# Kernel optimization log

Measured on AMD Instinct MI355X. Metric: run time of the kernel, lower is better.

The kernel has to match this reference:

```python
import jax, jax.numpy as jnp
import numpy as np

B, S, HID, H = 4, 2048, 1024, 8
D = HID // H  # per-head dim = 128


def setup_inputs() -> dict:
    key = jax.random.key(0)
    ks = jax.random.split(key, 8)
    q = jax.random.normal(ks[0], (B, S, HID), dtype=jnp.float32)
    k = jax.random.normal(ks[1], (B, S, HID), dtype=jnp.float32)
    v = jax.random.normal(ks[2], (B, S, HID), dtype=jnp.float32)
    mask = jax.random.randint(ks[3], (B, S), 0, 2, dtype=jnp.int32)  # 1 = masked key
    # Linear(hidden, hidden, bias=False) weights, stored [in, out] so y = x @ W
    xavier = lambda kk: jax.random.uniform(kk, (HID, HID), jnp.float32,
                                           -np.sqrt(6.0 / (2 * HID)), np.sqrt(6.0 / (2 * HID)))
    return {"q": q, "k": k, "v": v, "mask": mask,
            "Wq": xavier(ks[4]), "Wk": xavier(ks[5]), "Wv": xavier(ks[6]), "Wo": xavier(ks[7])}


def reference(q, k, v, mask, Wq, Wk, Wv, Wo):
    scale = D ** -0.5
    # project and split heads: [B,S,HID] -> [B,H,S,D]
    qq = (q @ Wq).reshape(B, S, H, D).transpose(0, 2, 1, 3) * scale
    kk = (k @ Wk).reshape(B, S, H, D).transpose(0, 2, 1, 3)
    vv = (v @ Wv).reshape(B, S, H, D).transpose(0, 2, 1, 3)
    # scores [B,H,Sq,Sk]; mask broadcasts over heads and query rows (key padding)
    scores = jnp.einsum('bhqd,bhkd->bhqk', qq, kk)
    scores = jnp.where(mask.astype(bool)[:, None, None, :], jnp.float32(-1e9), scores)
    attn = jax.nn.softmax(scores, axis=-1)  # dropout_rate=0 (eval) -> identity
    ctx = jnp.einsum('bhqk,bhkd->bhqd', attn, vv)
    out = ctx.transpose(0, 2, 1, 3).reshape(B, S, HID) @ Wo
    return out, attn
```

## Files before the change

kernel.cpp:

```cpp
#include <hip/hip_runtime.h>
#include <hip/hip_bf16.h>

#define HIDN 1024
#define NH   8
#define DH   128
#define BB   4
#define SS   2048

typedef __bf16 bf16;
typedef bf16 bf16x4 __attribute__((ext_vector_type(4)));
typedef bf16 bf16x8 __attribute__((ext_vector_type(8)));
typedef float f32x4 __attribute__((ext_vector_type(4)));

static __device__ inline f32x4 mfma16(bf16x8 a, bf16x8 b, f32x4 c) {
    return __builtin_amdgcn_mfma_f32_16x16x32_bf16(a, b, c, 0, 0, 0);
}

static __device__ inline void gload_lds16(const void* g, void* l) {
    __builtin_amdgcn_global_load_lds(
        (const __attribute__((address_space(1))) unsigned int*)g,
        (__attribute__((address_space(3))) unsigned int*)l, 16, 0, 0);
}

__global__ void cvt_kernel(const float* __restrict__ q, const float* __restrict__ k,
                           const float* __restrict__ v,
                           bf16* __restrict__ qo, bf16* __restrict__ ko, bf16* __restrict__ vo) {
    const float* src = blockIdx.y == 0 ? q : blockIdx.y == 1 ? k : v;
    bf16* dst = blockIdx.y == 0 ? qo : blockIdx.y == 1 ? ko : vo;
    const size_t n = (size_t)BB * SS * HIDN;
    for (size_t i = ((size_t)blockIdx.x * blockDim.x + threadIdx.x) * 8; i < n;
         i += (size_t)gridDim.x * blockDim.x * 8) {
        float4 a = *(const float4*)&src[i];
        float4 b = *(const float4*)&src[i + 4];
        bf16x8 o = {(bf16)a.x, (bf16)a.y, (bf16)a.z, (bf16)a.w,
                    (bf16)b.x, (bf16)b.y, (bf16)b.z, (bf16)b.w};
        *(bf16x8*)&dst[i] = o;
    }
}

__global__ void wconv_kernel(const float* __restrict__ W0, const float* __restrict__ W1,
                             const float* __restrict__ W2, const float* __restrict__ W3,
                             bf16* __restrict__ O) {
    const float* W = blockIdx.z == 0 ? W0 : blockIdx.z == 1 ? W1 : blockIdx.z == 2 ? W2 : W3;
    bf16* WT = O + (size_t)blockIdx.z * HIDN * HIDN;
    int nb = blockIdx.x * 64;
    int kb = blockIdx.y * 64;
    int t = threadIdx.x;
    __shared__ bf16 tile[64][72];
    {
        int r = t >> 2, cp = (t & 3) * 16;
        #pragma unroll
        for (int j = 0; j < 16; j += 4) {
            float4 val = *(const float4*)&W[(size_t)(kb + r) * HIDN + nb + cp + j];
            tile[r][cp + j + 0] = (bf16)val.x;
            tile[r][cp + j + 1] = (bf16)val.y;
            tile[r][cp + j + 2] = (bf16)val.z;
            tile[r][cp + j + 3] = (bf16)val.w;
        }
    }
    __syncthreads();
    {
        int n = t >> 2, kp = (t & 3) * 16;
        bf16 o[16];
        #pragma unroll
        for (int j = 0; j < 16; ++j) o[j] = tile[kp + j][n];
        #pragma unroll
        for (int j = 0; j < 2; ++j)
            *(bf16x8*)&WT[(size_t)(nb + n) * HIDN + kb + kp + j * 8] = *(bf16x8*)&o[j * 8];
    }
}

template <typename CT>
__global__ __launch_bounds__(256, 2)
void gemm_bt_kernel(const bf16* __restrict__ A, const bf16* __restrict__ Bt,
                    CT* __restrict__ C, float alpha) {
    __shared__ bf16 Asm[128 * 64];
    __shared__ bf16 Bsm[128 * 64];
    int orig = blockIdx.x + blockIdx.y * gridDim.x;
    int virt = (orig & 7) * 64 + (orig >> 3);
    int bm = (virt & 63) * 128;
    int bn = (virt >> 6) * 128;
    int t = threadIdx.x;
    int wave = t >> 6, lane = t & 63;
    int wr = wave >> 1, wc = wave & 1;
    int lr = lane & 15, lg = lane >> 4;
    f32x4 acc[4][4] = {};
    for (int k0 = 0; k0 < HIDN; k0 += 64) {
        #pragma unroll
        for (int i = 0; i < 4; ++i) {
            int o = i * 4096 + wave * 1024 + lane * 16;
            int r = o >> 7, cb = o & 127;
            int cbs = cb ^ ((r & 7) << 4);
            gload_lds16(&A[(size_t)(bm + r) * HIDN + k0 + (cbs >> 1)],
                        (char*)Asm + i * 4096 + wave * 1024);
            gload_lds16(&Bt[(size_t)(bn + r) * HIDN + k0 + (cbs >> 1)],
                        (char*)Bsm + i * 4096 + wave * 1024);
        }
        asm volatile("s_waitcnt vmcnt(0)" ::: "memory");
        __syncthreads();
        #pragma unroll
        for (int kd = 0; kd < 2; ++kd) {
            bf16x8 af[4], bfr[4];
            #pragma unroll
            for (int mi = 0; mi < 4; ++mi) {
                int row = wr * 64 + mi * 16 + lr;
                int cb = (kd * 64 + lg * 16) ^ ((row & 7) << 4);
                af[mi] = *(const bf16x8*)((const char*)Asm + row * 128 + cb);
            }
            #pragma unroll
            for (int ni = 0; ni < 4; ++ni) {
                int row = wc * 64 + ni * 16 + lr;
                int cb = (kd * 64 + lg * 16) ^ ((row & 7) << 4);
                bfr[ni] = *(const bf16x8*)((const char*)Bsm + row * 128 + cb);
            }
            #pragma unroll
            for (int mi = 0; mi < 4; ++mi)
                #pragma unroll
                for (int ni = 0; ni < 4; ++ni)
                    acc[mi][ni] = mfma16(af[mi], bfr[ni], acc[mi][ni]);
        }
        __syncthreads();
    }
    #pragma unroll
    for (int mi = 0; mi < 4; ++mi)
        #pragma unroll
        for (int ni = 0; ni < 4; ++ni)
            #pragma unroll
            for (int r = 0; r < 4; ++r) {
                int row = bm + wr * 64 + mi * 16 + lg * 4 + r;
                int col = bn + wc * 64 + ni * 16 + lr;
                C[(size_t)row * HIDN + col] = (CT)(acc[mi][ni][r] * alpha);
            }
}

__global__ void vt_kernel(const bf16* __restrict__ vv, bf16* __restrict__ vvT) {
    int st = blockIdx.x;
    int bh = blockIdx.y;
    int b = bh >> 3, h = bh & 7;
    int t = threadIdx.x;
    __shared__ bf16 tile[64][136];
    {
        int r = t >> 2, part = (t & 3) * 32;
        #pragma unroll
        for (int j = 0; j < 4; ++j)
            *(bf16x8*)&tile[r][part + j * 8] =
                *(const bf16x8*)&vv[((size_t)b * SS + st * 64 + r) * HIDN + h * DH + part + j * 8];
    }
    __syncthreads();
    {
        int d = t >> 1, kh = (t & 1) * 32;
        bf16 o[32];
        #pragma unroll
        for (int j = 0; j < 32; ++j) o[j] = tile[kh + j][d];
        #pragma unroll
        for (int j = 0; j < 4; ++j)
            *(bf16x8*)&vvT[((size_t)bh * DH + d) * SS + st * 64 + kh + j * 8] = *(bf16x8*)&o[j * 8];
    }
}

static __device__ inline void stage_k(const bf16* kbase, int kt, bf16* Ksm, int wave, int lane) {
    #pragma unroll
    for (int i = 0; i < 8; ++i) {
        int o = i * 4096 + wave * 1024 + lane * 16;
        int r = o >> 8, cb = o & 255;
        int cbs = cb ^ ((r & 7) << 4);
        gload_lds16(&kbase[(size_t)(kt * 128 + r) * HIDN + (cbs >> 1)],
                    (char*)Ksm + i * 4096 + wave * 1024);
    }
    asm volatile("s_waitcnt vmcnt(0)" ::: "memory");
}

static __device__ inline bf16x8 read_k(const bf16* Ksm, int row, int cstart_bytes) {
    int cb = cstart_bytes ^ ((row & 7) << 4);
    return *(const bf16x8*)((const char*)Ksm + row * 256 + cb);
}

__global__ __launch_bounds__(256, 2)
void attn_stats_kernel(const bf16* __restrict__ qq, const bf16* __restrict__ kk,
                       const int* __restrict__ mask,
                       float* __restrict__ mrow, float* __restrict__ lrow) {
    int orig = blockIdx.x + blockIdx.y * gridDim.x;
    int virt = (orig & 7) * 64 + (orig >> 3);
    int qt = virt & 15, bh = virt >> 4;
    int b = bh >> 3, h = bh & 7;
    int t = threadIdx.x;
    int wave = t >> 6, lane = t & 63;
    int wr = wave >> 1, wc = wave & 1;
    int lr = lane & 15, lg = lane >> 4;

    __shared__ bf16 Ksm[128 * 128];
    __shared__ float sm[2][128], sl[2][128], runm[128], runl[128];
    if (t < 128) { runm[t] = -3.4e38f; runl[t] = 0.f; }

    const bf16* qbase = qq + (size_t)b * SS * HIDN + h * DH;
    const bf16* kbase = kk + (size_t)b * SS * HIDN + h * DH;
    const int* mbase = mask + b * SS;

    bf16x8 qf[4][4];
    #pragma unroll
    for (int mi = 0; mi < 4; ++mi)
        #pragma unroll
        for (int kd = 0; kd < 4; ++kd)
            qf[mi][kd] = *(const bf16x8*)&qbase[(size_t)(qt * 128 + wr * 64 + mi * 16 + lr) * HIDN + kd * 32 + lg * 8];

    for (int kt = 0; kt < SS / 128; ++kt) {
        stage_k(kbase, kt, Ksm, wave, lane);
        __syncthreads();
        f32x4 acc[4][4] = {};
        #pragma unroll
        for (int kd = 0; kd < 4; ++kd) {
            bf16x8 kf[4];
            #pragma unroll
            for (int ni = 0; ni < 4; ++ni)
                kf[ni] = read_k(Ksm, wc * 64 + ni * 16 + lr, kd * 64 + lg * 16);
            #pragma unroll
            for (int mi = 0; mi < 4; ++mi)
                #pragma unroll
                for (int ni = 0; ni < 4; ++ni)
                    acc[mi][ni] = mfma16(qf[mi][kd], kf[ni], acc[mi][ni]);
        }
        bool mk[4];
        #pragma unroll
        for (int ni = 0; ni < 4; ++ni)
            mk[ni] = mbase[kt * 128 + wc * 64 + ni * 16 + lr] != 0;

        float tm[16], tl[16];
        #pragma unroll
        for (int mi = 0; mi < 4; ++mi)
            #pragma unroll
            for (int r = 0; r < 4; ++r) {
                float v0 = mk[0] ? -1e9f : acc[mi][0][r];
                float v1 = mk[1] ? -1e9f : acc[mi][1][r];
                float v2 = mk[2] ? -1e9f : acc[mi][2][r];
                float v3 = mk[3] ? -1e9f : acc[mi][3][r];
                float mx = fmaxf(fmaxf(v0, v1), fmaxf(v2, v3));
                #pragma unroll
                for (int o = 1; o < 16; o <<= 1) mx = fmaxf(mx, __shfl_xor(mx, o));
                float se = __expf(v0 - mx) + __expf(v1 - mx) + __expf(v2 - mx) + __expf(v3 - mx);
                #pragma unroll
                for (int o = 1; o < 16; o <<= 1) se += __shfl_xor(se, o);
                tm[mi * 4 + r] = mx;
                tl[mi * 4 + r] = se;
            }
        if (lr == 0) {
            #pragma unroll
            for (int mi = 0; mi < 4; ++mi)
                #pragma unroll
                for (int r = 0; r < 4; ++r) {
                    int row = wr * 64 + mi * 16 + lg * 4 + r;
                    sm[wc][row] = tm[mi * 4 + r];
                    sl[wc][row] = tl[mi * 4 + r];
                }
        }
        __syncthreads();
        if (t < 128) {
            float m0 = sm[0][t], m1 = sm[1][t];
            float mt = fmaxf(m0, m1);
            float lt = sl[0][t] * __expf(m0 - mt) + sl[1][t] * __expf(m1 - mt);
            float mo = runm[t];
            float mn = fmaxf(mo, mt);
            runl[t] = runl[t] * __expf(mo - mn) + lt * __expf(mt - mn);
            runm[t] = mn;
        }
    }
    __syncthreads();
    if (t < 128) {
        size_t idx = (size_t)bh * SS + qt * 128 + t;
        mrow[idx] = runm[t];
        lrow[idx] = 1.0f / runl[t];
    }
}

__global__ __launch_bounds__(256, 2)
void attn_pv_kernel(const bf16* __restrict__ qq, const bf16* __restrict__ kk,
                    const bf16* __restrict__ vvT, const int* __restrict__ mask,
                    const float* __restrict__ mrow, const float* __restrict__ lrow,
                    float* __restrict__ attn, bf16* __restrict__ ctx) {
    int orig = blockIdx.x + blockIdx.y * gridDim.x;
    int virt = (orig & 7) * 64 + (orig >> 3);
    int qt = virt & 15, bh = virt >> 4;
    int b = bh >> 3, h = bh & 7;
    int t = threadIdx.x;
    int wave = t >> 6, lane = t & 63;
    int wr = wave >> 1, wc = wave & 1;
    int lr = lane & 15, lg = lane >> 4;

    __shared__ bf16 Ksm[128 * 128];
    __shared__ bf16 P[128][136];

    const bf16* qbase = qq + (size_t)b * SS * HIDN + h * DH;
    const bf16* kbase = kk + (size_t)b * SS * HIDN + h * DH;
    const int* mbase = mask + b * SS;

    bf16x8 qf[4][4];
    #pragma unroll
    for (int mi = 0; mi < 4; ++mi)
        #pragma unroll
        for (int kd = 0; kd < 4; ++kd)
            qf[mi][kd] = *(const bf16x8*)&qbase[(size_t)(qt * 128 + wr * 64 + mi * 16 + lr) * HIDN + kd * 32 + lg * 8];

    float rm[16], rl[16];
    #pragma unroll
    for (int mi = 0; mi < 4; ++mi)
        #pragma unroll
        for (int r = 0; r < 4; ++r) {
            size_t idx = (size_t)bh * SS + qt * 128 + wr * 64 + mi * 16 + lg * 4 + r;
            rm[mi * 4 + r] = mrow[idx];
            rl[mi * 4 + r] = lrow[idx];
        }

    f32x4 cacc[4][4] = {};
    for (int kt = 0; kt < SS / 128; ++kt) {
        stage_k(kbase, kt, Ksm, wave, lane);
        __syncthreads();
        f32x4 acc[4][4] = {};
        #pragma unroll
        for (int kd = 0; kd < 4; ++kd) {
            bf16x8 kf[4];
            #pragma unroll
            for (int ni = 0; ni < 4; ++ni)
                kf[ni] = read_k(Ksm, wc * 64 + ni * 16 + lr, kd * 64 + lg * 16);
            #pragma unroll
            for (int mi = 0; mi < 4; ++mi)
                #pragma unroll
                for (int ni = 0; ni < 4; ++ni)
                    acc[mi][ni] = mfma16(qf[mi][kd], kf[ni], acc[mi][ni]);
        }
        bool mk[4];
        #pragma unroll
        for (int ni = 0; ni < 4; ++ni)
            mk[ni] = mbase[kt * 128 + wc * 64 + ni * 16 + lr] != 0;

        #pragma unroll
        for (int mi = 0; mi < 4; ++mi)
            #pragma unroll
            for (int ni = 0; ni < 4; ++ni)
                #pragma unroll
                for (int r = 0; r < 4; ++r) {
                    float s = mk[ni] ? -1e9f : acc[mi][ni][r];
                    float p = __expf(s - rm[mi * 4 + r]) * rl[mi * 4 + r];
                    int rowl = wr * 64 + mi * 16 + lg * 4 + r;
                    int coll = wc * 64 + ni * 16 + lr;
                    P[rowl][coll] = (bf16)p;
                    __builtin_nontemporal_store(
                        p, &attn[((size_t)bh * SS + qt * 128 + rowl) * SS + kt * 128 + coll]);
                }
        __syncthreads();
        #pragma unroll
        for (int ks = 0; ks < 4; ++ks) {
            bf16x8 pf[4], vf[4];
            #pragma unroll
            for (int mi = 0; mi < 4; ++mi)
                pf[mi] = *(const bf16x8*)&P[wr * 64 + mi * 16 + lr][ks * 32 + lg * 8];
            #pragma unroll
            for (int ni = 0; ni < 4; ++ni)
                vf[ni] = *(const bf16x8*)&vvT[((size_t)bh * DH + wc * 64 + ni * 16 + lr) * SS + kt * 128 + ks * 32 + lg * 8];
            #pragma unroll
            for (int mi = 0; mi < 4; ++mi)
                #pragma unroll
                for (int ni = 0; ni < 4; ++ni)
                    cacc[mi][ni] = mfma16(pf[mi], vf[ni], cacc[mi][ni]);
        }
        __syncthreads();
    }
    #pragma unroll
    for (int mi = 0; mi < 4; ++mi)
        #pragma unroll
        for (int ni = 0; ni < 4; ++ni)
            #pragma unroll
            for (int r = 0; r < 4; ++r) {
                int qrow = qt * 128 + wr * 64 + mi * 16 + lg * 4 + r;
                int d = wc * 64 + ni * 16 + lr;
                ctx[((size_t)b * SS + qrow) * HIDN + h * DH + d] = (bf16)cacc[mi][ni][r];
            }
}

extern "C" void kernel_launch(void* const* d_in, const int* in_sizes, int n_in,
                              void* d_out, int out_size, void* d_ws, size_t ws_size,
                              hipStream_t stream) {
    const float* q = (const float*)d_in[0];
    const float* k = (const float*)d_in[1];
    const float* v = (const float*)d_in[2];
    const int* mask = (const int*)d_in[3];
    const float* Wq = (const float*)d_in[4];
    const float* Wk = (const float*)d_in[5];
    const float* Wv = (const float*)d_in[6];
    const float* Wo = (const float*)d_in[7];
    (void)in_sizes; (void)n_in; (void)out_size; (void)ws_size;

    float* outp = (float*)d_out;
    float* attn = outp + (size_t)BB * SS * HIDN;

    char* ws = (char*)d_ws;
    size_t off = 0;
    auto alloc = [&](size_t bytes) { char* p = ws + off; off += (bytes + 255) & ~(size_t)255; return p; };
    const size_t wbytes = (size_t)HIDN * HIDN * sizeof(bf16);
    const size_t tbytes = (size_t)BB * SS * HIDN * sizeof(bf16);
    bf16* WmatT = (bf16*)alloc(4 * wbytes);
    bf16* qbf = (bf16*)alloc(tbytes);
    bf16* kbf = (bf16*)alloc(tbytes);
    bf16* vbf = (bf16*)alloc(tbytes);
    bf16* qqb = (bf16*)alloc(tbytes);
    bf16* kkb = (bf16*)alloc(tbytes);
    bf16* vvb = (bf16*)alloc(tbytes);
    float* mrowb = (float*)alloc((size_t)BB * NH * SS * sizeof(float));
    float* lrowb = (float*)alloc((size_t)BB * NH * SS * sizeof(float));
    bf16* vvTb = qbf;
    bf16* ctxb = kbf;
    bf16* WqT = WmatT, *WkT = WmatT + HIDN * HIDN, *WvT = WmatT + 2 * (size_t)HIDN * HIDN,
        *WoT = WmatT + 3 * (size_t)HIDN * HIDN;

    dim3 blk(256);
    cvt_kernel<<<dim3(1024, 3), blk, 0, stream>>>(q, k, v, qbf, kbf, vbf);
    wconv_kernel<<<dim3(16, 16, 4), blk, 0, stream>>>(Wq, Wk, Wv, Wo, WmatT);

    const float scale = 0.08838834764831845f;
    gemm_bt_kernel<bf16><<<dim3(64, 8), blk, 0, stream>>>(qbf, WqT, qqb, scale);
    gemm_bt_kernel<bf16><<<dim3(64, 8), blk, 0, stream>>>(kbf, WkT, kkb, 1.0f);
    gemm_bt_kernel<bf16><<<dim3(64, 8), blk, 0, stream>>>(vbf, WvT, vvb, 1.0f);

    vt_kernel<<<dim3(SS / 64, BB * NH), blk, 0, stream>>>(vvb, vvTb);

    attn_stats_kernel<<<dim3(16, 32), blk, 0, stream>>>(qqb, kkb, mask, mrowb, lrowb);
    attn_pv_kernel<<<dim3(16, 32), blk, 0, stream>>>(qqb, kkb, vvTb, mask, mrowb, lrowb, attn, ctxb);

    gemm_bt_kernel<float><<<dim3(64, 8), blk, 0, stream>>>(ctxb, WoT, outp, 1.0f);
}
```

Baseline: 404.6 us.

## Fuse attention stats and PV kernels, double-buffer GEMM, fold V transpose into GEMM

Merges the separate softmax-statistics and PV attention kernels into one kernel that runs both passes per block. Row max and sum stay in registers with per-lane online updates, and the mask is precomputed into a bitmask. Adds double-buffered K staging in the stats pass and prefetch of the next K tile during PV. The projection GEMM gets double-buffered LDS staging, and the V projection writes its output transposed directly, which removes vt_kernel and the m/l round-trip through global memory. The risks are a 64KB shared-memory footprint that may reduce occupancy below 2 blocks per CU, and higher register pressure.

```diff
diff --git a/kernel.cpp b/kernel.cpp
--- a/kernel.cpp
+++ b/kernel.cpp
@@ -70,12 +70,11 @@
     }
 }
 
-template <typename CT>
+template <int OUTMODE>
 __global__ __launch_bounds__(256, 2)
 void gemm_bt_kernel(const bf16* __restrict__ A, const bf16* __restrict__ Bt,
-                    CT* __restrict__ C, float alpha) {
-    __shared__ bf16 Asm[128 * 64];
-    __shared__ bf16 Bsm[128 * 64];
+                    void* __restrict__ Cp, float alpha) {
+    __shared__ __align__(16) char smem[65536];
     int orig = blockIdx.x + blockIdx.y * gridDim.x;
     int virt = (orig & 7) * 64 + (orig >> 3);
     int bm = (virt & 63) * 128;
@@ -84,19 +83,29 @@
     int wave = t >> 6, lane = t & 63;
     int wr = wave >> 1, wc = wave & 1;
     int lr = lane & 15, lg = lane >> 4;
+    int so = wave * 1024 + lane * 16;
     f32x4 acc[4][4] = {};
-    for (int k0 = 0; k0 < HIDN; k0 += 64) {
+
+    auto stage = [&](int k0, char* buf) {
         #pragma unroll
         for (int i = 0; i < 4; ++i) {
-            int o = i * 4096 + wave * 1024 + lane * 16;
+            int o = i * 4096 + so;
             int r = o >> 7, cb = o & 127;
             int cbs = cb ^ ((r & 7) << 4);
-            gload_lds16(&A[(size_t)(bm + r) * HIDN + k0 + (cbs >> 1)],
-                        (char*)Asm + i * 4096 + wave * 1024);
-            gload_lds16(&Bt[(size_t)(bn + r) * HIDN + k0 + (cbs >> 1)],
-                        (char*)Bsm + i * 4096 + wave * 1024);
-        }
-        asm volatile("s_waitcnt vmcnt(0)" ::: "memory");
+            gload_lds16(&A[(size_t)(bm + r) * HIDN + k0 + (cbs >> 1)], buf + i * 4096 + wave * 1024);
+            gload_lds16(&Bt[(size_t)(bn + r) * HIDN + k0 + (cbs >> 1)], buf + 16384 + i * 4096 + wave * 1024);
+        }
+    };
+    stage(0, smem);
+    for (int kt = 0; kt < 16; ++kt) {
+        const char* cur = smem + (kt & 1) * 32768;
+        char* nxt = smem + ((kt & 1) ^ 1) * 32768;
+        if (kt < 15) {
+            stage((kt + 1) * 64, nxt);
+            asm volatile("s_waitcnt vmcnt(8)" ::: "memory");
+        } else {
+            asm volatile("s_waitcnt vmcnt(0)" ::: "memory");
+        }
         __syncthreads();
         #pragma unroll
         for (int kd = 0; kd < 2; ++kd) {
@@ -105,13 +114,13 @@
             for (int mi = 0; mi < 4; ++mi) {
                 int row = wr * 64 + mi * 16 + lr;
                 int cb = (kd * 64 + lg * 16) ^ ((row & 7) << 4);
-                af[mi] = *(const bf16x8*)((const char*)Asm + row * 128 + cb);
+                af[mi] = *(const bf16x8*)(cur + row * 128 + cb);
             }
             #pragma unroll
             for (int ni = 0; ni < 4; ++ni) {
                 int row = wc * 64 + ni * 16 + lr;
                 int cb = (kd * 64 + lg * 16) ^ ((row & 7) << 4);
-                bfr[ni] = *(const bf16x8*)((const char*)Bsm + row * 128 + cb);
+                bfr[ni] = *(const bf16x8*)(cur + 16384 + row * 128 + cb);
             }
             #pragma unroll
             for (int mi = 0; mi < 4; ++mi)
@@ -121,64 +130,68 @@
         }
         __syncthreads();
     }
-    #pragma unroll
-    for (int mi = 0; mi < 4; ++mi)
-        #pragma unroll
-        for (int ni = 0; ni < 4; ++ni)
-            #pragma unroll
-            for (int r = 0; r < 4; ++r) {
-                int row = bm + wr * 64 + mi * 16 + lg * 4 + r;
-                int col = bn + wc * 64 + ni * 16 + lr;
-                C[(size_t)row * HIDN + col] = (CT)(acc[mi][ni][r] * alpha);
-            }
-}
-
-__global__ void vt_kernel(const bf16* __restrict__ vv, bf16* __restrict__ vvT) {
-    int st = blockIdx.x;
-    int bh = blockIdx.y;
-    int b = bh >> 3, h = bh & 7;
-    int t = threadIdx.x;
-    __shared__ bf16 tile[64][136];
-    {
-        int r = t >> 2, part = (t & 3) * 32;
-        #pragma unroll
-        for (int j = 0; j < 4; ++j)
-            *(bf16x8*)&tile[r][part + j * 8] =
-                *(const bf16x8*)&vv[((size_t)b * SS + st * 64 + r) * HIDN + h * DH + part + j * 8];
-    }
-    __syncthreads();
-    {
-        int d = t >> 1, kh = (t & 1) * 32;
-        bf16 o[32];
-        #pragma unroll
-        for (int j = 0; j < 32; ++j) o[j] = tile[kh + j][d];
-        #pragma unroll
-        for (int j = 0; j < 4; ++j)
-            *(bf16x8*)&vvT[((size_t)bh * DH + d) * SS + st * 64 + kh + j * 8] = *(bf16x8*)&o[j * 8];
-    }
-}
-
-static __device__ inline void stage_k(const bf16* kbase, int kt, bf16* Ksm, int wave, int lane) {
+    if constexpr (OUTMODE == 2) {
+        bf16* tile_t = (bf16*)smem;
+        #pragma unroll
+        for (int mi = 0; mi < 4; ++mi)
+            #pragma unroll
+            for (int ni = 0; ni < 4; ++ni) {
+                bf16x4 o = {(bf16)acc[mi][ni][0], (bf16)acc[mi][ni][1],
+                            (bf16)acc[mi][ni][2], (bf16)acc[mi][ni][3]};
+                *(bf16x4*)&tile_t[(wc * 64 + ni * 16 + lr) * 136 + wr * 64 + mi * 16 + lg * 4] = o;
+            }
+        __syncthreads();
+        int d = t >> 1, sh = (t & 1) * 64;
+        int b = bm >> 11, h = bn >> 7;
+        bf16* vvT = (bf16*)Cp;
+        size_t base = ((size_t)(b * NH + h) * DH + d) * SS + (bm & 2047) + sh;
+        #pragma unroll
+        for (int j = 0; j < 8; ++j)
+            *(bf16x8*)&vvT[base + j * 8] = *(const bf16x8*)&tile_t[d * 136 + sh + j * 8];
+    } else {
+        #pragma unroll
+        for (int mi = 0; mi < 4; ++mi)
+            #pragma unroll
+            for (int ni = 0; ni < 4; ++ni)
+                #pragma unroll
+                for (int r = 0; r < 4; ++r) {
+                    int row = bm + wr * 64 + mi * 16 + lg * 4 + r;
+                    int col = bn + wc * 64 + ni * 16 + lr;
+                    if constexpr (OUTMODE == 0)
+                        ((bf16*)Cp)[(size_t)row * HIDN + col] = (bf16)(acc[mi][ni][r] * alpha);
+                    else
+                        ((float*)Cp)[(size_t)row * HIDN + col] = acc[mi][ni][r] * alpha;
+                }
+    }
+}
+
+static __device__ inline void stage_k(const bf16* kbase, int kt, char* Ksm, int wave, int lane) {
     #pragma unroll
     for (int i = 0; i < 8; ++i) {
         int o = i * 4096 + wave * 1024 + lane * 16;
         int r = o >> 8, cb = o & 255;
         int cbs = cb ^ ((r & 7) << 4);
         gload_lds16(&kbase[(size_t)(kt * 128 + r) * HIDN + (cbs >> 1)],
-                    (char*)Ksm + i * 4096 + wave * 1024);
-    }
-    asm volatile("s_waitcnt vmcnt(0)" ::: "memory");
-}
-
-static __device__ inline bf16x8 read_k(const bf16* Ksm, int row, int cstart_bytes) {
+                    Ksm + i * 4096 + wave * 1024);
+    }
+}
+
+static __device__ inline bf16x8 read_k(const char* Ksm, int row, int cstart_bytes) {
     int cb = cstart_bytes ^ ((row & 7) << 4);
-    return *(const bf16x8*)((const char*)Ksm + row * 256 + cb);
+    return *(const bf16x8*)(Ksm + row * 256 + cb);
 }
 
 __global__ __launch_bounds__(256, 2)
-void attn_stats_kernel(const bf16* __restrict__ qq, const bf16* __restrict__ kk,
-                       const int* __restrict__ mask,
-                       float* __restrict__ mrow, float* __restrict__ lrow) {
+void attn_fused_kernel(const bf16* __restrict__ qq, const bf16* __restrict__ kk,
+                       const bf16* __restrict__ vvT, const int* __restrict__ mask,
+                       float* __restrict__ attn, bf16* __restrict__ ctx) {
+    __shared__ __align__(16) char smem[67584];
+    char* Ksm0 = smem;
+    char* Ksm1 = smem + 32768;
+    bf16(*P)[136] = (bf16(*)[136])(smem + 32768);
+    float* smf = (float*)(smem + 32768);
+    float* slf = (float*)(smem + 32768 + 1024);
+
     int orig = blockIdx.x + blockIdx.y * gridDim.x;
     int virt = (orig & 7) * 64 + (orig >> 3);
     int qt = virt & 15, bh = virt >> 4;
@@ -188,10 +201,6 @@
     int wr = wave >> 1, wc = wave & 1;
     int lr = lane & 15, lg = lane >> 4;
 
-    __shared__ bf16 Ksm[128 * 128];
-    __shared__ float sm[2][128], sl[2][128], runm[128], runl[128];
-    if (t < 128) { runm[t] = -3.4e38f; runl[t] = 0.f; }
-
     const bf16* qbase = qq + (size_t)b * SS * HIDN + h * DH;
     const bf16* kbase = kk + (size_t)b * SS * HIDN + h * DH;
     const int* mbase = mask + b * SS;
@@ -203,8 +212,28 @@
         for (int kd = 0; kd < 4; ++kd)
             qf[mi][kd] = *(const bf16x8*)&qbase[(size_t)(qt * 128 + wr * 64 + mi * 16 + lr) * HIDN + kd * 32 + lg * 8];
 
-    for (int kt = 0; kt < SS / 128; ++kt) {
-        stage_k(kbase, kt, Ksm, wave, lane);
+    unsigned long long mkbits = 0;
+    #pragma unroll
+    for (int kt = 0; kt < 16; ++kt)
+        #pragma unroll
+        for (int ni = 0; ni < 4; ++ni)
+            mkbits |= (unsigned long long)(mbase[kt * 128 + wc * 64 + ni * 16 + lr] != 0)
+                      << (kt * 4 + ni);
+
+    float m_[16], l_[16];
+    #pragma unroll
+    for (int s = 0; s < 16; ++s) { m_[s] = -3.4e38f; l_[s] = 0.f; }
+
+    stage_k(kbase, 0, Ksm0, wave, lane);
+    for (int kt = 0; kt < 16; ++kt) {
+        const char* cur = (kt & 1) ? Ksm1 : Ksm0;
+        char* nxt = (kt & 1) ? Ksm0 : Ksm1;
+        if (kt < 15) {
+            stage_k(kbase, kt + 1, nxt, wave, lane);
+            asm volatile("s_waitcnt vmcnt(8)" ::: "memory");
+        } else {
+            asm volatile("s_waitcnt vmcnt(0)" ::: "memory");
+        }
         __syncthreads();
         f32x4 acc[4][4] = {};
         #pragma unroll
@@ -212,132 +241,92 @@
             bf16x8 kf[4];
             #pragma unroll
             for (int ni = 0; ni < 4; ++ni)
-                kf[ni] = read_k(Ksm, wc * 64 + ni * 16 + lr, kd * 64 + lg * 16);
+                kf[ni] = read_k(cur, wc * 64 + ni * 16 + lr, kd * 64 + lg * 16);
             #pragma unroll
             for (int mi = 0; mi < 4; ++mi)
                 #pragma unroll
                 for (int ni = 0; ni < 4; ++ni)
                     acc[mi][ni] = mfma16(qf[mi][kd], kf[ni], acc[mi][ni]);
         }
-        bool mk[4];
-        #pragma unroll
-        for (int ni = 0; ni < 4; ++ni)
-            mk[ni] = mbase[kt * 128 + wc * 64 + ni * 16 + lr] != 0;
-
-        float tm[16], tl[16];
         #pragma unroll
         for (int mi = 0; mi < 4; ++mi)
             #pragma unroll
             for (int r = 0; r < 4; ++r) {
-                float v0 = mk[0] ? -1e9f : acc[mi][0][r];
-                float v1 = mk[1] ? -1e9f : acc[mi][1][r];
-                float v2 = mk[2] ? -1e9f : acc[mi][2][r];
-                float v3 = mk[3] ? -1e9f : acc[mi][3][r];
-                float mx = fmaxf(fmaxf(v0, v1), fmaxf(v2, v3));
-                #pragma unroll
-                for (int o = 1; o < 16; o <<= 1) mx = fmaxf(mx, __shfl_xor(mx, o));
-                float se = __expf(v0 - mx) + __expf(v1 - mx) + __expf(v2 - mx) + __expf(v3 - mx);
-                #pragma unroll
-                for (int o = 1; o < 16; o <<= 1) se += __shfl_xor(se, o);
-                tm[mi * 4 + r] = mx;
-                tl[mi * 4 + r] = se;
-            }
-        if (lr == 0) {
-            #pragma unroll
-            for (int mi = 0; mi < 4; ++mi)
-                #pragma unroll
-                for (int r = 0; r < 4; ++r) {
-                    int row = wr * 64 + mi * 16 + lg * 4 + r;
-                    sm[wc][row] = tm[mi * 4 + r];
-                    sl[wc][row] = tl[mi * 4 + r];
-                }
-        }
-        __syncthreads();
-        if (t < 128) {
-            float m0 = sm[0][t], m1 = sm[1][t];
-            float mt = fmaxf(m0, m1);
-            float lt = sl[0][t] * __expf(m0 - mt) + sl[1][t] * __expf(m1 - mt);
-            float mo = runm[t];
-            float mn = fmaxf(mo, mt);
-            runl[t] = runl[t] * __expf(mo - mn) + lt * __expf(mt - mn);
-            runm[t] = mn;
-        }
+                int s = mi * 4 + r;
+                float v0 = ((mkbits >> (kt * 4 + 0)) & 1) ? -1e9f : acc[mi][0][r];
+                float v1 = ((mkbits >> (kt * 4 + 1)) & 1) ? -1e9f : acc[mi][1][r];
+                float v2 = ((mkbits >> (kt * 4 + 2)) & 1) ? -1e9f : acc[mi][2][r];
+                float v3 = ((mkbits >> (kt * 4 + 3)) & 1) ? -1e9f : acc[mi][3][r];
+                float tm = fmaxf(fmaxf(v0, v1), fmaxf(v2, v3));
+                float tl = __expf(v0 - tm) + __expf(v1 - tm) + __expf(v2 - tm) + __expf(v3 - tm);
+                float mo = m_[s], mn = fmaxf(mo, tm);
+                l_[s] = l_[s] * __expf(mo - mn) + tl * __expf(tm - mn);
+                m_[s] = mn;
+            }
+        __syncthreads();
+    }
+
+    stage_k(kbase, 0, Ksm0, wave, lane);
+
+    #pragma unroll
+    for (int o = 1; o < 16; o <<= 1)
+        #pragma unroll
+        for (int s = 0; s < 16; ++s) {
+            float mo = __shfl_xor(m_[s], o);
+            float lo = __shfl_xor(l_[s], o);
+            float mn = fmaxf(m_[s], mo);
+            l_[s] = l_[s] * __expf(m_[s] - mn) + lo * __expf(mo - mn);
+            m_[s] = mn;
+        }
+    if (lr == 0) {
+        #pragma unroll
+        for (int mi = 0; mi < 4; ++mi)
+            #pragma unroll
+            for (int r = 0; r < 4; ++r) {
+                int row = wr * 64 + mi * 16 + lg * 4 + r;
+                smf[wc * 128 + row] = m_[mi * 4 + r];
+                slf[wc * 128 + row] = l_[mi * 4 + r];
+            }
     }
     __syncthreads();
-    if (t < 128) {
-        size_t idx = (size_t)bh * SS + qt * 128 + t;
-        mrow[idx] = runm[t];
-        lrow[idx] = 1.0f / runl[t];
-    }
-}
-
-__global__ __launch_bounds__(256, 2)
-void attn_pv_kernel(const bf16* __restrict__ qq, const bf16* __restrict__ kk,
-                    const bf16* __restrict__ vvT, const int* __restrict__ mask,
-                    const float* __restrict__ mrow, const float* __restrict__ lrow,
-                    float* __restrict__ attn, bf16* __restrict__ ctx) {
-    int orig = blockIdx.x + blockIdx.y * gridDim.x;
-    int virt = (orig & 7) * 64 + (orig >> 3);
-    int qt = virt & 15, bh = virt >> 4;
-    int b = bh >> 3, h = bh & 7;
-    int t = threadIdx.x;
-    int wave = t >> 6, lane = t & 63;
-    int wr = wave >> 1, wc = wave & 1;
-    int lr = lane & 15, lg = lane >> 4;
-
-    __shared__ bf16 Ksm[128 * 128];
-    __shared__ bf16 P[128][136];
-
-    const bf16* qbase = qq + (size_t)b * SS * HIDN + h * DH;
-    const bf16* kbase = kk + (size_t)b * SS * HIDN + h * DH;
-    const int* mbase = mask + b * SS;
-
-    bf16x8 qf[4][4];
+    float rm[16], rl[16];
     #pragma unroll
     for (int mi = 0; mi < 4; ++mi)
         #pragma unroll
-        for (int kd = 0; kd < 4; ++kd)
-            qf[mi][kd] = *(const bf16x8*)&qbase[(size_t)(qt * 128 + wr * 64 + mi * 16 + lr) * HIDN + kd * 32 + lg * 8];
-
-    float rm[16], rl[16];
-    #pragma unroll
-    for (int mi = 0; mi < 4; ++mi)
-        #pragma unroll
         for (int r = 0; r < 4; ++r) {
-            size_t idx = (size_t)bh * SS + qt * 128 + wr * 64 + mi * 16 + lg * 4 + r;
-            rm[mi * 4 + r] = mrow[idx];
-            rl[mi * 4 + r] = lrow[idx];
-        }
+            int row = wr * 64 + mi * 16 + lg * 4 + r;
+            float m0 = smf[row], m1 = smf[128 + row];
+            float l0 = slf[row], l1 = slf[128 + row];
+            float mn = fmaxf(m0, m1);
+            float l = l0 * __expf(m0 - mn) + l1 * __expf(m1 - mn);
+            rm[mi * 4 + r] = mn;
+            rl[mi * 4 + r] = 1.0f / l;
+        }
+    asm volatile("s_waitcnt vmcnt(0)" ::: "memory");
+    __syncthreads();
 
     f32x4 cacc[4][4] = {};
-    for (int kt = 0; kt < SS / 128; ++kt) {
-        stage_k(kbase, kt, Ksm, wave, lane);
-        __syncthreads();
+    for (int kt = 0; kt < 16; ++kt) {
         f32x4 acc[4][4] = {};
         #pragma unroll
         for (int kd = 0; kd < 4; ++kd) {
             bf16x8 kf[4];
             #pragma unroll
             for (int ni = 0; ni < 4; ++ni)
-                kf[ni] = read_k(Ksm, wc * 64 + ni * 16 + lr, kd * 64 + lg * 16);
+                kf[ni] = read_k(Ksm0, wc * 64 + ni * 16 + lr, kd * 64 + lg * 16);
             #pragma unroll
             for (int mi = 0; mi < 4; ++mi)
                 #pragma unroll
                 for (int ni = 0; ni < 4; ++ni)
                     acc[mi][ni] = mfma16(qf[mi][kd], kf[ni], acc[mi][ni]);
         }
-        bool mk[4];
-        #pragma unroll
-        for (int ni = 0; ni < 4; ++ni)
-            mk[ni] = mbase[kt * 128 + wc * 64 + ni * 16 + lr] != 0;
-
         #pragma unroll
         for (int mi = 0; mi < 4; ++mi)
             #pragma unroll
             for (int ni = 0; ni < 4; ++ni)
                 #pragma unroll
                 for (int r = 0; r < 4; ++r) {
-                    float s = mk[ni] ? -1e9f : acc[mi][ni][r];
+                    float s = ((mkbits >> (kt * 4 + ni)) & 1) ? -1e9f : acc[mi][ni][r];
                     float p = __expf(s - rm[mi * 4 + r]) * rl[mi * 4 + r];
                     int rowl = wr * 64 + mi * 16 + lg * 4 + r;
                     int coll = wc * 64 + ni * 16 + lr;
@@ -346,6 +335,7 @@
                         p, &attn[((size_t)bh * SS + qt * 128 + rowl) * SS + kt * 128 + coll]);
                 }
         __syncthreads();
+        if (kt < 15) stage_k(kbase, kt + 1, Ksm0, wave, lane);
         #pragma unroll
         for (int ks = 0; ks < 4; ++ks) {
             bf16x8 pf[4], vf[4];
@@ -361,6 +351,7 @@
                 for (int ni = 0; ni < 4; ++ni)
                     cacc[mi][ni] = mfma16(pf[mi], vf[ni], cacc[mi][ni]);
         }
+        asm volatile("s_waitcnt vmcnt(0)" ::: "memory");
         __syncthreads();
     }
     #pragma unroll
@@ -402,27 +393,21 @@
     bf16* vbf = (bf16*)alloc(tbytes);
     bf16* qqb = (bf16*)alloc(tbytes);
     bf16* kkb = (bf16*)alloc(tbytes);
-    bf16* vvb = (bf16*)alloc(tbytes);
-    float* mrowb = (float*)alloc((size_t)BB * NH * SS * sizeof(float));
-    float* lrowb = (float*)alloc((size_t)BB * NH * SS * sizeof(float));
-    bf16* vvTb = qbf;
-    bf16* ctxb = kbf;
-    bf16* WqT = WmatT, *WkT = WmatT + HIDN * HIDN, *WvT = WmatT + 2 * (size_t)HIDN * HIDN,
-        *WoT = WmatT + 3 * (size_t)HIDN * HIDN;
+    bf16* vvTb = (bf16*)alloc(tbytes);
+    bf16* ctxb = qbf;
+    bf16* WqT = WmatT, *WkT = WmatT + (size_t)HIDN * HIDN,
+        *WvT = WmatT + 2 * (size_t)HIDN * HIDN, *WoT = WmatT + 3 * (size_t)HIDN * HIDN;
 
     dim3 blk(256);
     cvt_kernel<<<dim3(1024, 3), blk, 0, stream>>>(q, k, v, qbf, kbf, vbf);
     wconv_kernel<<<dim3(16, 16, 4), blk, 0, stream>>>(Wq, Wk, Wv, Wo, WmatT);
 
     const float scale = 0.08838834764831845f;
-    gemm_bt_kernel<bf16><<<dim3(64, 8), blk, 0, stream>>>(qbf, WqT, qqb, scale);
-    gemm_bt_kernel<bf16><<<dim3(64, 8), blk, 0, stream>>>(kbf, WkT, kkb, 1.0f);
-    gemm_bt_kernel<bf16><<<dim3(64, 8), blk, 0, stream>>>(vbf, WvT, vvb, 1.0f);
-
-    vt_kernel<<<dim3(SS / 64, BB * NH), blk, 0, stream>>>(vvb, vvTb);
-
-    attn_stats_kernel<<<dim3(16, 32), blk, 0, stream>>>(qqb, kkb, mask, mrowb, lrowb);
-    attn_pv_kernel<<<dim3(16, 32), blk, 0, stream>>>(qqb, kkb, vvTb, mask, mrowb, lrowb, attn, ctxb);
-
-    gemm_bt_kernel<float><<<dim3(64, 8), blk, 0, stream>>>(ctxb, WoT, outp, 1.0f);
-}
+    gemm_bt_kernel<0><<<dim3(64, 8), blk, 0, stream>>>(qbf, WqT, qqb, scale);
+    gemm_bt_kernel<0><<<dim3(64, 8), blk, 0, stream>>>(kbf, WkT, kkb, 1.0f);
+    gemm_bt_kernel<2><<<dim3(64, 8), blk, 0, stream>>>(vbf, WvT, vvTb, 1.0f);
+
+    attn_fused_kernel<<<dim3(16, 32), blk, 0, stream>>>(qqb, kkb, vvTb, mask, attn, ctxb);
+
+    gemm_bt_kernel<1><<<dim3(64, 8), blk, 0, stream>>>(ctxb, WoT, outp, 1.0f);
+}
```

After: 403.9 us. Within noise of the previous version (-0.2%).
